# Optimization experiments

Measured on AMD Instinct MI355X. Metric: run time of the kernel, lower is better.

The kernel has to match this reference:

```python
import jax, jax.numpy as jnp
import numpy as np

C = 2000        # num_classes
D_FEAT = 2048   # memory feature dim (hardcoded in module)
N_V = 20000     # rgb samples
N_I = 20000     # ir samples
T = 1.0
PRED_W, FEAT_W, CONF_W = 0.45, 0.4, 0.15
OT_REG, OT_ITERS = 0.07, 30
HIGH_TH, MID_TH, TOPK = 0.55, 0.25, 3


def setup_inputs() -> dict:
    key = jax.random.key(0)
    k = jax.random.split(key, 6)
    return {
        "vis_logits": jax.random.normal(k[0], (N_V, C), jnp.float32),
        "ir_logits": jax.random.normal(k[1], (N_I, C), jnp.float32),
        "vis_memory": jax.random.normal(k[2], (C, D_FEAT), jnp.float32),
        "ir_memory": jax.random.normal(k[3], (C, D_FEAT), jnp.float32),
        "rgb_ids": jax.random.randint(k[4], (N_V,), 0, C),
        "ir_ids": jax.random.randint(k[5], (N_I,), 0, C),
    }


def _class_stats(scores, labels):
    # per-class mean of softmax scores + entropy (matches _build_class_stats)
    proto_sum = jax.ops.segment_sum(scores, labels, num_segments=C)      # [C, C]
    counts = jax.ops.segment_sum(jnp.ones((scores.shape[0],), scores.dtype), labels, num_segments=C)
    proto = proto_sum / jnp.clip(counts, 1.0)[:, None]
    p = jnp.clip(proto, 1e-12)
    entropy = -(p * jnp.log(p)).sum(axis=1)
    return proto, counts, entropy, counts > 0


def _sinkhorn(cost, a, b, mask_f):
    kernel = jnp.exp(-cost / max(OT_REG, 1e-4)) * mask_f
    eps = 1e-8
    def body(_, uv):
        u, v = uv
        kv = kernel @ v + eps
        u = jnp.where(a > 0, a / kv, 0.0)
        ktu = kernel.T @ u + eps
        v = jnp.where(b > 0, b / ktu, 0.0)
        return (u, v)
    u, v = jax.lax.fori_loop(0, OT_ITERS, body, (jnp.ones_like(a), jnp.ones_like(b)))
    return u[:, None] * kernel * v[None, :] * mask_f


def _topk_mask(m):
    k = min(TOPK, m.shape[1])
    vals, idx = jax.lax.top_k(m, k)
    rows = jnp.arange(m.shape[0])[:, None]
    return jnp.zeros_like(m).at[rows, idx].set(vals)


def reference(vis_logits, ir_logits, vis_memory, ir_memory, rgb_ids, ir_ids):
    # save() in 'scores' mode: temperature softmax
    vis_scores = jax.nn.softmax(T * vis_logits, axis=1)
    ir_scores = jax.nn.softmax(T * ir_logits, axis=1)

    vis_proto, vis_count, vis_ent, vis_active = _class_stats(vis_scores, rgb_ids)
    ir_proto, ir_count, ir_ent, ir_active = _class_stats(ir_scores, ir_ids)

    vmem = vis_memory / jnp.clip(jnp.linalg.norm(vis_memory, axis=1, keepdims=True), 1e-12)
    imem = ir_memory / jnp.clip(jnp.linalg.norm(ir_memory, axis=1, keepdims=True), 1e-12)
    feat_score = jnp.clip((vmem @ imem.T + 1.0) * 0.5, 0.0, 1.0)          # [C, C]
    pred_score = 0.5 * (vis_proto + ir_proto.T)
    conf_score = jnp.clip(
        1.0 - (vis_ent[:, None] + ir_ent[None, :]) / (2.0 * np.log(C + 1e-12)), 0.0, 1.0)

    active = vis_active[:, None] & ir_active[None, :]
    cost = PRED_W * (1.0 - pred_score) + FEAT_W * (1.0 - feat_score) + CONF_W * (1.0 - conf_score)
    masked_max = jnp.max(jnp.where(active, cost, -jnp.inf))
    high = jnp.where(active.any(), masked_max + 1.0, 1.0)
    cost = jnp.where(active, cost, high)

    a = vis_count / jnp.clip(vis_count.sum(), 1.0)
    b = ir_count / jnp.clip(ir_count.sum(), 1.0)
    transport = _sinkhorn(cost, a, b, active.astype(cost.dtype))

    row_t = transport / jnp.clip(transport.sum(axis=1, keepdims=True), 1e-12)
    col_t = transport.T / jnp.clip(transport.T.sum(axis=1, keepdims=True), 1e-12)
    row_conf = row_t.max(axis=1); row_assign = row_t.argmax(axis=1)
    col_conf = col_t.max(axis=1); col_assign = col_t.argmax(axis=1)

    ids = jnp.arange(C)
    mutual_rows = col_assign[row_assign] == ids
    mutual_cols = row_assign[col_assign] == ids
    common_row = vis_active & (row_conf >= HIGH_TH) & mutual_rows
    common_col = ir_active & (col_conf >= HIGH_TH) & mutual_cols
    spec_row = vis_active & (row_conf >= HIGH_TH) & ~common_row
    rem_row = vis_active & (row_conf >= MID_TH) & (row_conf < HIGH_TH)
    rem_col = ir_active & (col_conf >= MID_TH) & (col_conf < HIGH_TH)

    common_rm = jnp.where(common_row[:, None],
                          jax.nn.one_hot(row_assign, C, dtype=row_t.dtype) * row_conf[:, None],
                          0.0)
    specific_rm = row_t * spec_row[:, None].astype(row_t.dtype)
    remain_rm = _topk_mask(row_t * rem_row[:, None].astype(row_t.dtype))
    remain_col_rm = _topk_mask(col_t * rem_col[:, None].astype(col_t.dtype))

    return jnp.stack([row_t, col_t, common_rm, specific_rm, remain_rm, remain_col_rm])
```

## Files before the change

### kernel.cpp

```cpp
#include <hip/hip_runtime.h>

#define CN 2000
#define DF 2048
#define NS 20000
#define NBLK 250
#define NGRP 25
#define GRPSZ 10

typedef __attribute__((ext_vector_type(4))) float          f32x4;
typedef __attribute__((ext_vector_type(4))) int            i32x4;
typedef __attribute__((ext_vector_type(4))) unsigned short u16x4;

__device__ __forceinline__ float wredSum(float v){
#pragma unroll
  for (int o = 32; o >= 1; o >>= 1) v += __shfl_xor(v, o, 64);
  return v;
}
__device__ __forceinline__ float wredMax(float v){
#pragma unroll
  for (int o = 32; o >= 1; o >>= 1) v = fmaxf(v, __shfl_xor(v, o, 64));
  return v;
}
__device__ __forceinline__ unsigned short bfbits(float x){
  union { float f; unsigned u; } c; c.f = x;
  return (unsigned short)((c.u + 0x7fffu + ((c.u >> 16) & 1u)) >> 16);
}
__device__ __forceinline__ void gload16(const void* g, void* lds){
  __builtin_amdgcn_global_load_lds((const __attribute__((address_space(1))) unsigned int*)g,
      (__attribute__((address_space(3))) unsigned int*)lds, 16, 0, 0);
}

__device__ __forceinline__ void gbar(int* bar, int target){
  asm volatile("s_waitcnt vmcnt(0)" ::: "memory");
  __syncthreads();
  if (threadIdx.x == 0){
    int g = blockIdx.x / GRPSZ;
    int prev = __hip_atomic_fetch_add(&bar[64 + g * 32], 1,
                  __ATOMIC_RELAXED, __HIP_MEMORY_SCOPE_AGENT);
    if (prev == target * GRPSZ - 1){
      int rp = __hip_atomic_fetch_add(&bar[0], 1,
                  __ATOMIC_RELAXED, __HIP_MEMORY_SCOPE_AGENT);
      if (rp == target * NGRP - 1){
        __hip_atomic_store(&bar[32], target, __ATOMIC_RELAXED, __HIP_MEMORY_SCOPE_AGENT);
      }
    }
    while (__hip_atomic_load(&bar[32], __ATOMIC_RELAXED, __HIP_MEMORY_SCOPE_AGENT) < target){
      __builtin_amdgcn_s_sleep(2);
    }
  }
  __syncthreads();
}

__global__ void k_zero(int* p, int n, int* bar){
  int i = blockIdx.x * 256 + threadIdx.x;
  if (i < n) p[i] = 0;
  if (i < 1024) bar[i] = 0;
}

__global__ void k_hist(const int* __restrict__ rgb, const int* __restrict__ iri,
                       int* cv, int* ci){
  int i = blockIdx.x * 256 + threadIdx.x;
  if (i < NS) atomicAdd(&cv[rgb[i]], 1);
  else if (i < 2 * NS) atomicAdd(&ci[iri[i - NS]], 1);
}

__global__ __launch_bounds__(1024) void k_scan(const int* __restrict__ cv, const int* __restrict__ ci,
                                               int* ov, int* oi){
  __shared__ int s[2048];
  int t = threadIdx.x;
  for (int pass = 0; pass < 2; ++pass){
    const int* c = pass ? ci : cv;
    int* o = pass ? oi : ov;
    s[t] = (t < CN) ? c[t] : 0;
    s[t + 1024] = (t + 1024 < CN) ? c[t + 1024] : 0;
    __syncthreads();
    for (int off = 1; off < 2048; off <<= 1){
      int a = (t >= off) ? s[t - off] : 0;
      int b = (t + 1024 >= off) ? s[t + 1024 - off] : 0;
      __syncthreads();
      s[t] += a; s[t + 1024] += b;
      __syncthreads();
    }
    if (t < CN) o[t] = s[t] - c[t];
    if (t + 1024 < CN) o[t + 1024] = s[t + 1024] - c[t + 1024];
    __syncthreads();
  }
}

__global__ void k_scatter(const int* __restrict__ rgb, const int* __restrict__ iri,
                          const int* __restrict__ ov, const int* __restrict__ oi,
                          int* curv, int* curi, int* ordv, int* ordi){
  int i = blockIdx.x * 256 + threadIdx.x;
  if (i < NS){
    int l = rgb[i];
    int p = atomicAdd(&curv[l], 1);
    ordv[ov[l] + p] = i;
  } else if (i < 2 * NS){
    int k = i - NS;
    int l = iri[k];
    int p = atomicAdd(&curi[l], 1);
    ordi[oi[l] + p] = k;
  }
}

__global__ __launch_bounds__(256) void k_class(const float* __restrict__ visl, const float* __restrict__ irl,
    const int* __restrict__ cv, const int* __restrict__ ci,
    const int* __restrict__ ov, const int* __restrict__ oi,
    const int* __restrict__ ordv, const int* __restrict__ ordi,
    float* __restrict__ pv, float* __restrict__ pi_,
    float* __restrict__ ev, float* __restrict__ ei){
  __shared__ __attribute__((aligned(16))) float acc4[4][2048];
  __shared__ int mem[128];
  __shared__ float red[4];
  int t = threadIdx.x, w = t >> 6, l = t & 63;
  bool ir = (blockIdx.x >= CN);
  int c = ir ? blockIdx.x - CN : blockIdx.x;
  const float* logits = ir ? irl : visl;
  int n = (ir ? ci : cv)[c];
  int base = (ir ? oi : ov)[c];
  const int* ord = ir ? ordi : ordv;
  float* proto = ir ? pi_ : pv;
  float* ent = ir ? ei : ev;
  bool useL = (n <= 128);
  for (int m = t; m < n && m < 128; m += 256) mem[m] = ord[base + m];
  for (int j = t; j < 2048; j += 256){
    acc4[0][j] = 0.f; acc4[1][j] = 0.f; acc4[2][j] = 0.f; acc4[3][j] = 0.f;
  }
  __syncthreads();
  if (t == 0 && useL){
    for (int a = 1; a < n; ++a){
      int key = mem[a]; int b = a - 1;
      while (b >= 0 && mem[b] > key){ mem[b + 1] = mem[b]; --b; }
      mem[b + 1] = key;
    }
  }
  __syncthreads();
  for (int m = w; m < n; m += 4){
    int sidx = useL ? mem[m] : ord[base + m];
    const f32x4* row = (const f32x4*)(logits + (size_t)sidx * CN);
    f32x4 x[8]; float mx = -3.0e38f;
#pragma unroll
    for (int k = 0; k < 8; ++k){
      int idx = l + k * 64;
      f32x4 vv = {-3.0e38f, -3.0e38f, -3.0e38f, -3.0e38f};
      if (idx < 500) vv = row[idx];
      x[k] = vv;
      mx = fmaxf(mx, fmaxf(fmaxf(vv[0], vv[1]), fmaxf(vv[2], vv[3])));
    }
    mx = wredMax(mx);
    float sm = 0.f;
#pragma unroll
    for (int k = 0; k < 8; ++k){
      int idx = l + k * 64;
      if (idx < 500){
        f32x4 e;
        e[0] = expf(x[k][0] - mx); e[1] = expf(x[k][1] - mx);
        e[2] = expf(x[k][2] - mx); e[3] = expf(x[k][3] - mx);
        x[k] = e;
        sm += e[0] + e[1] + e[2] + e[3];
      }
    }
    sm = wredSum(sm);
    float inv = 1.f / sm;
#pragma unroll
    for (int k = 0; k < 8; ++k){
      int idx = l + k * 64;
      if (idx < 500){
        f32x4* a = (f32x4*)&acc4[w][idx * 4];
        f32x4 cur = *a;
        cur[0] += x[k][0] * inv; cur[1] += x[k][1] * inv;
        cur[2] += x[k][2] * inv; cur[3] += x[k][3] * inv;
        *a = cur;
      }
    }
  }
  __syncthreads();
  float invc = 1.f / fmaxf((float)n, 1.f);
  float el = 0.f;
  for (int j = t; j < CN; j += 256){
    float p = (acc4[0][j] + acc4[1][j] + acc4[2][j] + acc4[3][j]) * invc;
    proto[(size_t)c * CN + j] = p;
    p = fmaxf(p, 1e-12f);
    el -= p * logf(p);
  }
  el = wredSum(el);
  if (l == 0) red[w] = el;
  __syncthreads();
  if (t == 0) ent[c] = red[0] + red[1] + red[2] + red[3];
}

__global__ __launch_bounds__(256) void k_conv(const float* __restrict__ vm, const float* __restrict__ im,
    unsigned short* __restrict__ vmb, unsigned short* __restrict__ imb,
    float* __restrict__ rv, float* __restrict__ ri){
  int g = blockIdx.x * 256 + threadIdx.x;
  int wid = g >> 6, l = g & 63;
  if (wid >= 2 * CN) return;
  const float* src = (wid < CN) ? vm : im;
  unsigned short* dst = (wid < CN) ? vmb : imb;
  int r = (wid < CN) ? wid : wid - CN;
  const f32x4* row = (const f32x4*)(src + (size_t)r * DF);
  float s = 0.f;
#pragma unroll
  for (int k = 0; k < 8; ++k){
    int idx = l + k * 64;
    f32x4 vv = row[idx];
    s += vv[0]*vv[0] + vv[1]*vv[1] + vv[2]*vv[2] + vv[3]*vv[3];
    u16x4 o;
    o[0] = bfbits(vv[0]); o[1] = bfbits(vv[1]); o[2] = bfbits(vv[2]); o[3] = bfbits(vv[3]);
    *(u16x4*)(dst + (size_t)r * DF + idx * 4) = o;
  }
  s = wredSum(s);
  if (l == 0) ((wid < CN) ? rv : ri)[r] = 1.f / fmaxf(sqrtf(s), 1e-12f);
}

__global__ __launch_bounds__(256) void k_prep(const float* __restrict__ pv, const float* __restrict__ pi_,
    const float* __restrict__ ev, const float* __restrict__ ei,
    const int* __restrict__ cv, const int* __restrict__ ci, float* __restrict__ E){
  __shared__ float s[64][65];
  int t = threadIdx.x;
  int i0 = blockIdx.y * 64, j0 = blockIdx.x * 64;
#pragma unroll
  for (int rr = 0; rr < 4; ++rr){
    int jl = (t >> 4) + rr * 16;
    int ch = t & 15;
    int gj = j0 + jl;
    int gib = i0 + ch * 4;
    f32x4 vv = {0.f, 0.f, 0.f, 0.f};
    if (gj < CN){
      if (gib + 3 < CN) vv = *(const f32x4*)(pi_ + (size_t)gj * CN + gib);
      else {
        for (int q = 0; q < 4; ++q) if (gib + q < CN) vv[q] = pi_[(size_t)gj * CN + gib + q];
      }
    }
    s[ch*4+0][jl] = vv[0]; s[ch*4+1][jl] = vv[1]; s[ch*4+2][jl] = vv[2]; s[ch*4+3][jl] = vv[3];
  }
  __syncthreads();
#pragma unroll
  for (int rr = 0; rr < 4; ++rr){
    int il = (t >> 4) + rr * 16;
    int ch = t & 15;
    int gi = i0 + il;
    int gjb = j0 + ch * 4;
    if (gi >= CN) continue;
    f32x4 pvv = {0.f, 0.f, 0.f, 0.f};
    bool full = (gjb + 3 < CN);
    if (full) pvv = *(const f32x4*)(pv + (size_t)gi * CN + gjb);
    else { for (int q = 0; q < 4; ++q) if (gjb + q < CN) pvv[q] = pv[(size_t)gi * CN + gjb + q]; }
    float evi = ev[gi];
    bool avi = cv[gi] > 0;
    f32x4 o;
#pragma unroll
    for (int q = 0; q < 4; ++q){
      int gj = gjb + q;
      if (gj >= CN){ o[q] = 0.f; continue; }
      float pred = 0.5f * (pvv[q] + s[il][ch*4+q]);
      float conf = fminf(fmaxf(1.f - (evi + ei[gj]) / 15.201804919084164f, 0.f), 1.f);
      float base = 0.45f * (1.f - pred) + 0.15f * (1.f - conf);
      bool act = avi && (ci[gj] > 0);
      o[q] = act ? expf(-base / 0.07f) : 0.f;
    }
    if (full) *(f32x4*)(E + (size_t)gi * CN + gjb) = o;
    else { for (int q = 0; q < 4; ++q) if (gjb + q < CN) E[(size_t)gi * CN + gjb + q] = o[q]; }
  }
}

__global__ __launch_bounds__(256) void k_gemm2(const unsigned short* __restrict__ Ag,
    const unsigned short* __restrict__ Bg, const float* __restrict__ rv,
    const float* __restrict__ ri, const float* __restrict__ E, float* __restrict__ Km){
  __shared__ __attribute__((aligned(16))) unsigned short As[128 * 64];
  __shared__ __attribute__((aligned(16))) unsigned short Bs[128 * 64];
  int t = threadIdx.x, w = t >> 6, l = t & 63;
  int i0 = blockIdx.y * 128, j0 = blockIdx.x * 128;
  int wm = w >> 1, wn = w & 1;
  int srow8 = l >> 3, sch = l & 7;
  int lr = l & 15, hk = l >> 4;
  f32x4 z = {0.f, 0.f, 0.f, 0.f};
  f32x4 acc[4][4];
#pragma unroll
  for (int a = 0; a < 4; ++a)
#pragma unroll
    for (int b = 0; b < 4; ++b) acc[a][b] = z;

  for (int kt = 0; kt < DF / 64; ++kt){
    int k0 = kt * 64;
#pragma unroll
    for (int c2 = 0; c2 < 4; ++c2){
      int rbase = c2 * 32 + w * 8;
      int row = rbase + srow8;
      int lch = sch ^ (srow8 & 7);
      int gi = i0 + row; if (gi > CN - 1) gi = CN - 1;
      int gj = j0 + row; if (gj > CN - 1) gj = CN - 1;
      gload16(Ag + (size_t)gi * DF + k0 + lch * 8, &As[rbase * 64]);
      gload16(Bg + (size_t)gj * DF + k0 + lch * 8, &Bs[rbase * 64]);
    }
    __syncthreads();
#pragma unroll
    for (int s2 = 0; s2 < 2; ++s2){
      i32x4 af[4], bf[4];
#pragma unroll
      for (int f2 = 0; f2 < 4; ++f2){
        int ar = wm * 64 + f2 * 16 + lr;
        int ac = (s2 * 4 + hk) ^ (ar & 7);
        af[f2] = *(const i32x4*)&As[ar * 64 + ac * 8];
        int br = wn * 64 + f2 * 16 + lr;
        int bc = (s2 * 4 + hk) ^ (br & 7);
        bf[f2] = *(const i32x4*)&Bs[br * 64 + bc * 8];
      }
#pragma unroll
      for (int a = 0; a < 4; ++a)
#pragma unroll
        for (int b = 0; b < 4; ++b)
          asm volatile("v_mfma_f32_16x16x32_bf16 %0, %1, %2, %0"
                       : "+v"(acc[a][b]) : "v"(af[a]), "v"(bf[b]));
    }
    __syncthreads();
  }
#pragma unroll
  for (int a = 0; a < 4; ++a){
    int ib = i0 + wm * 64 + a * 16 + hk * 4;
#pragma unroll
    for (int b = 0; b < 4; ++b){
      int j = j0 + wn * 64 + b * 16 + lr;
      if (j < CN){
        float rij = ri[j];
#pragma unroll
        for (int q = 0; q < 4; ++q){
          int i = ib + q;
          if (i < CN){
            float dot = acc[a][b][q] * rv[i] * rij;
            float feat = fminf(fmaxf((dot + 1.f) * 0.5f, 0.f), 1.f);
            float kv = E[(size_t)i * CN + j] * expf(-0.4f * (1.f - feat) / 0.07f);
            Km[(size_t)i * CN + j] = kv;
          }
        }
      }
    }
  }
}

__global__ __launch_bounds__(256) void k_tr(const float* __restrict__ Km, float* __restrict__ KT){
  __shared__ float s[64][65];
  int t = threadIdx.x;
  int i0 = blockIdx.y * 64, j0 = blockIdx.x * 64;
#pragma unroll
  for (int rr = 0; rr < 4; ++rr){
    int il = (t >> 4) + rr * 16;
    int ch = t & 15;
    int gi = i0 + il, gjb = j0 + ch * 4;
    f32x4 vv = {0.f, 0.f, 0.f, 0.f};
    if (gi < CN){
      if (gjb + 3 < CN) vv = *(const f32x4*)(Km + (size_t)gi * CN + gjb);
      else { for (int q = 0; q < 4; ++q) if (gjb + q < CN) vv[q] = Km[(size_t)gi * CN + gjb + q]; }
    }
    s[ch*4+0][il] = vv[0]; s[ch*4+1][il] = vv[1]; s[ch*4+2][il] = vv[2]; s[ch*4+3][il] = vv[3];
  }
  __syncthreads();
#pragma unroll
  for (int rr = 0; rr < 4; ++rr){
    int jl = (t >> 4) + rr * 16;
    int ch = t & 15;
    int gj = j0 + jl, gib = i0 + ch * 4;
    if (gj >= CN) continue;
    f32x4 o;
    o[0] = s[jl][ch*4+0]; o[1] = s[jl][ch*4+1]; o[2] = s[jl][ch*4+2]; o[3] = s[jl][ch*4+3];
    if (gib + 3 < CN) *(f32x4*)(KT + (size_t)gj * CN + gib) = o;
    else { for (int q = 0; q < 4; ++q) if (gib + q < CN) KT[(size_t)gj * CN + gib + q] = o[q]; }
  }
}

__global__ __launch_bounds__(256, 1) void k_sink(
    const float* __restrict__ Km, const float* __restrict__ KTm,
    const int* __restrict__ cv, const int* __restrict__ ci,
    float* __restrict__ u_g, float* __restrict__ v_g,
    float* __restrict__ o0, float* __restrict__ o1,
    float* __restrict__ rconf, float* __restrict__ cconf,
    int* __restrict__ rass, int* __restrict__ cass,
    int* bar){
  __shared__ __attribute__((aligned(16))) float u_lds[2000];
  __shared__ __attribute__((aligned(16))) float v_lds[2000];
  int b = blockIdx.x, t = threadIdx.x, w = t >> 6, l = t & 63;
  int r0 = b * 8 + w * 2, r1 = r0 + 1;
  f32x4 z4 = {0.f, 0.f, 0.f, 0.f};
  f32x4 kA0[8], kA1[8], kT0[8], kT1[8];
  {
    const f32x4* g0 = (const f32x4*)(Km + (size_t)r0 * CN);
    const f32x4* g1 = (const f32x4*)(Km + (size_t)r1 * CN);
    const f32x4* h0 = (const f32x4*)(KTm + (size_t)r0 * CN);
    const f32x4* h1 = (const f32x4*)(KTm + (size_t)r1 * CN);
#pragma unroll
    for (int k = 0; k < 8; ++k){
      int idx = l + k * 64;
      bool ok = idx < 500;
      kA0[k] = ok ? g0[idx] : z4;
      kA1[k] = ok ? g1[idx] : z4;
      kT0[k] = ok ? h0[idx] : z4;
      kT1[k] = ok ? h1[idx] : z4;
    }
  }
  float a0 = (float)cv[r0] / 20000.0f, a1 = (float)cv[r1] / 20000.0f;
  float b0 = (float)ci[r0] / 20000.0f, b1 = (float)ci[r1] / 20000.0f;

  {
    float s0 = 0.f, s1 = 0.f;
#pragma unroll
    for (int k = 0; k < 8; ++k){
      s0 += kA0[k][0] + kA0[k][1] + kA0[k][2] + kA0[k][3];
      s1 += kA1[k][0] + kA1[k][1] + kA1[k][2] + kA1[k][3];
    }
    s0 = wredSum(s0); s1 = wredSum(s1);
    if (l == 0){
      __hip_atomic_store(&u_g[r0], (a0 > 0.f) ? a0 / (s0 + 1e-8f) : 0.f,
                         __ATOMIC_RELAXED, __HIP_MEMORY_SCOPE_AGENT);
      __hip_atomic_store(&u_g[r1], (a1 > 0.f) ? a1 / (s1 + 1e-8f) : 0.f,
                         __ATOMIC_RELAXED, __HIP_MEMORY_SCOPE_AGENT);
    }
  }
  int tgt = 1;
  gbar(bar, tgt); ++tgt;
  {
    float tmp[8];
#pragma unroll
    for (int k = 0; k < 8; ++k){
      int idx = t + k * 256;
      tmp[k] = (idx < CN) ? __hip_atomic_load(&u_g[idx], __ATOMIC_RELAXED, __HIP_MEMORY_SCOPE_AGENT) : 0.f;
    }
#pragma unroll
    for (int k = 0; k < 8; ++k){ int idx = t + k * 256; if (idx < CN) u_lds[idx] = tmp[k]; }
  }
  __syncthreads();
  const f32x4* ul4 = (const f32x4*)u_lds;
  const f32x4* vl4 = (const f32x4*)v_lds;

  for (int it = 0; it < 30; ++it){
    {
      float s0 = 0.f, s1 = 0.f;
#pragma unroll
      for (int k = 0; k < 8; ++k){
        int idx = l + k * 64;
        if (idx < 500){
          f32x4 x = ul4[idx];
          s0 += kT0[k][0]*x[0] + kT0[k][1]*x[1] + kT0[k][2]*x[2] + kT0[k][3]*x[3];
          s1 += kT1[k][0]*x[0] + kT1[k][1]*x[1] + kT1[k][2]*x[2] + kT1[k][3]*x[3];
        }
      }
      s0 = wredSum(s0); s1 = wredSum(s1);
      if (l == 0){
        __hip_atomic_store(&v_g[r0], (b0 > 0.f) ? b0 / (s0 + 1e-8f) : 0.f,
                           __ATOMIC_RELAXED, __HIP_MEMORY_SCOPE_AGENT);
        __hip_atomic_store(&v_g[r1], (b1 > 0.f) ? b1 / (s1 + 1e-8f) : 0.f,
                           __ATOMIC_RELAXED, __HIP_MEMORY_SCOPE_AGENT);
      }
    }
    gbar(bar, tgt); ++tgt;
    {
      float tmp[8];
#pragma unroll
      for (int k = 0; k < 8; ++k){
        int idx = t + k * 256;
        tmp[k] = (idx < CN) ? __hip_atomic_load(&v_g[idx], __ATOMIC_RELAXED, __HIP_MEMORY_SCOPE_AGENT) : 0.f;
      }
#pragma unroll
      for (int k = 0; k < 8; ++k){ int idx = t + k * 256; if (idx < CN) v_lds[idx] = tmp[k]; }
    }
    __syncthreads();
    if (it < 29){
      {
        float s0 = 0.f, s1 = 0.f;
#pragma unroll
        for (int k = 0; k < 8; ++k){
          int idx = l + k * 64;
          if (idx < 500){
            f32x4 x = vl4[idx];
            s0 += kA0[k][0]*x[0] + kA0[k][1]*x[1] + kA0[k][2]*x[2] + kA0[k][3]*x[3];
            s1 += kA1[k][0]*x[0] + kA1[k][1]*x[1] + kA1[k][2]*x[2] + kA1[k][3]*x[3];
          }
        }
        s0 = wredSum(s0); s1 = wredSum(s1);
        if (l == 0){
          __hip_atomic_store(&u_g[r0], (a0 > 0.f) ? a0 / (s0 + 1e-8f) : 0.f,
                             __ATOMIC_RELAXED, __HIP_MEMORY_SCOPE_AGENT);
          __hip_atomic_store(&u_g[r1], (a1 > 0.f) ? a1 / (s1 + 1e-8f) : 0.f,
                             __ATOMIC_RELAXED, __HIP_MEMORY_SCOPE_AGENT);
        }
      }
      gbar(bar, tgt); ++tgt;
      {
        float tmp[8];
#pragma unroll
        for (int k = 0; k < 8; ++k){
          int idx = t + k * 256;
          tmp[k] = (idx < CN) ? __hip_atomic_load(&u_g[idx], __ATOMIC_RELAXED, __HIP_MEMORY_SCOPE_AGENT) : 0.f;
        }
#pragma unroll
        for (int k = 0; k < 8; ++k){ int idx = t + k * 256; if (idx < CN) u_lds[idx] = tmp[k]; }
      }
      __syncthreads();
    }
  }
  {
    float s0 = 0.f, s1 = 0.f;
#pragma unroll
    for (int k = 0; k < 8; ++k){
      int idx = l + k * 64;
      if (idx < 500){
        f32x4 x = vl4[idx];
        s0 += kA0[k][0]*x[0] + kA0[k][1]*x[1] + kA0[k][2]*x[2] + kA0[k][3]*x[3];
        s1 += kA1[k][0]*x[0] + kA1[k][1]*x[1] + kA1[k][2]*x[2] + kA1[k][3]*x[3];
      }
    }
    s0 = wredSum(s0); s1 = wredSum(s1);
    float uu0 = u_lds[r0], uu1 = u_lds[r1];
    float f0 = uu0 * (1.f / fmaxf(uu0 * s0, 1e-12f));
    float f1 = uu1 * (1.f / fmaxf(uu1 * s1, 1e-12f));
    float bm0 = -1e30f, bm1 = -1e30f; int bi0 = 1 << 30, bi1 = 1 << 30;
    f32x4* d0 = (f32x4*)(o0 + (size_t)r0 * CN);
    f32x4* d1 = (f32x4*)(o0 + (size_t)r1 * CN);
#pragma unroll
    for (int k = 0; k < 8; ++k){
      int idx = l + k * 64;
      if (idx < 500){
        f32x4 x = vl4[idx];
        f32x4 w0, w1;
#pragma unroll
        for (int q = 0; q < 4; ++q){
          w0[q] = f0 * kA0[k][q] * x[q];
          w1[q] = f1 * kA1[k][q] * x[q];
        }
        d0[idx] = w0; d1[idx] = w1;
#pragma unroll
        for (int q = 0; q < 4; ++q){
          int j = idx * 4 + q;
          if (w0[q] > bm0){ bm0 = w0[q]; bi0 = j; }
          if (w1[q] > bm1){ bm1 = w1[q]; bi1 = j; }
        }
      }
    }
#pragma unroll
    for (int o = 32; o >= 1; o >>= 1){
      float om = __shfl_xor(bm0, o, 64); int oi2 = __shfl_xor(bi0, o, 64);
      if (om > bm0 || (om == bm0 && oi2 < bi0)){ bm0 = om; bi0 = oi2; }
      float om1 = __shfl_xor(bm1, o, 64); int oi3 = __shfl_xor(bi1, o, 64);
      if (om1 > bm1 || (om1 == bm1 && oi3 < bi1)){ bm1 = om1; bi1 = oi3; }
    }
    if (l == 0){ rconf[r0] = bm0; rass[r0] = bi0; rconf[r1] = bm1; rass[r1] = bi1; }
  }
  {
    float s0 = 0.f, s1 = 0.f;
#pragma unroll
    for (int k = 0; k < 8; ++k){
      int idx = l + k * 64;
      if (idx < 500){
        f32x4 x = ul4[idx];
        s0 += kT0[k][0]*x[0] + kT0[k][1]*x[1] + kT0[k][2]*x[2] + kT0[k][3]*x[3];
        s1 += kT1[k][0]*x[0] + kT1[k][1]*x[1] + kT1[k][2]*x[2] + kT1[k][3]*x[3];
      }
    }
    s0 = wredSum(s0); s1 = wredSum(s1);
    float vv0 = v_lds[r0], vv1 = v_lds[r1];
    float f0 = vv0 * (1.f / fmaxf(vv0 * s0, 1e-12f));
    float f1 = vv1 * (1.f / fmaxf(vv1 * s1, 1e-12f));
    float bm0 = -1e30f, bm1 = -1e30f; int bi0 = 1 << 30, bi1 = 1 << 30;
    f32x4* d0 = (f32x4*)(o1 + (size_t)r0 * CN);
    f32x4* d1 = (f32x4*)(o1 + (size_t)r1 * CN);
#pragma unroll
    for (int k = 0; k < 8; ++k){
      int idx = l + k * 64;
      if (idx < 500){
        f32x4 x = ul4[idx];
        f32x4 w0, w1;
#pragma unroll
        for (int q = 0; q < 4; ++q){
          w0[q] = f0 * kT0[k][q] * x[q];
          w1[q] = f1 * kT1[k][q] * x[q];
        }
        d0[idx] = w0; d1[idx] = w1;
#pragma unroll
        for (int q = 0; q < 4; ++q){
          int j = idx * 4 + q;
          if (w0[q] > bm0){ bm0 = w0[q]; bi0 = j; }
          if (w1[q] > bm1){ bm1 = w1[q]; bi1 = j; }
        }
      }
    }
#pragma unroll
    for (int o = 32; o >= 1; o >>= 1){
      float om = __shfl_xor(bm0, o, 64); int oi2 = __shfl_xor(bi0, o, 64);
      if (om > bm0 || (om == bm0 && oi2 < bi0)){ bm0 = om; bi0 = oi2; }
      float om1 = __shfl_xor(bm1, o, 64); int oi3 = __shfl_xor(bi1, o, 64);
      if (om1 > bm1 || (om1 == bm1 && oi3 < bi1)){ bm1 = om1; bi1 = oi3; }
    }
    if (l == 0){ cconf[r0] = bm0; cass[r0] = bi0; cconf[r1] = bm1; cass[r1] = bi1; }
  }
}

__global__ __launch_bounds__(256) void k_fill(const float* __restrict__ rt,
    const int* __restrict__ cv, const float* __restrict__ rc,
    const int* __restrict__ ra, const int* __restrict__ ca,
    float* o2, float* o3, float* o4, float* o5){
  int i = blockIdx.x, t = threadIdx.x;
  bool av = cv[i] > 0;
  float cval = rc[i]; int aidx = ra[i];
  bool high = av && (cval >= 0.55f);
  bool cm = high && (ca[aidx] == i);
  bool sp = high && !cm;
  f32x4 z = {0.f, 0.f, 0.f, 0.f};
  f32x4* p2 = (f32x4*)(o2 + (size_t)i * CN);
  f32x4* p3 = (f32x4*)(o3 + (size_t)i * CN);
  f32x4* p4 = (f32x4*)(o4 + (size_t)i * CN);
  f32x4* p5 = (f32x4*)(o5 + (size_t)i * CN);
  const f32x4* rp = (const f32x4*)(rt + (size_t)i * CN);
  for (int c = t; c < 500; c += 256){
    p2[c] = z;
    p3[c] = sp ? rp[c] : z;
    p4[c] = z;
    p5[c] = z;
  }
  __syncthreads();
  if (t == 0 && cm) o2[(size_t)i * CN + aidx] = cval;
}

__global__ __launch_bounds__(256) void k_topk(const float* __restrict__ rt, const float* __restrict__ ct,
    const int* __restrict__ cv, const int* __restrict__ ci,
    const float* __restrict__ rc, const float* __restrict__ cc,
    float* o4, float* o5){
  __shared__ float sv[256 * 3];
  __shared__ int si[256 * 3];
  int b = blockIdx.x;
  bool colp = (b >= CN);
  int r = colp ? b - CN : b;
  bool act = colp ? (ci[r] > 0) : (cv[r] > 0);
  float cf = colp ? cc[r] : rc[r];
  if (!(act && cf >= 0.25f && cf < 0.55f)) return;
  const float* M = colp ? ct : rt;
  float* o = colp ? o5 : o4;
  int t = threadIdx.x;
  float v0 = -1.f, v1 = -1.f, v2 = -1.f;
  int i0 = 1 << 30, i1 = 1 << 30, i2 = 1 << 30;
  for (int k = 0; k < 8; ++k){
    int j = t + k * 256;
    if (j >= CN) break;
    float val = M[(size_t)r * CN + j];
    if (val > v0 || (val == v0 && j < i0)){ v2=v1; i2=i1; v1=v0; i1=i0; v0=val; i0=j; }
    else if (val > v1 || (val == v1 && j < i1)){ v2=v1; i2=i1; v1=val; i1=j; }
    else if (val > v2 || (val == v2 && j < i2)){ v2=val; i2=j; }
  }
  sv[t*3+0]=v0; sv[t*3+1]=v1; sv[t*3+2]=v2;
  si[t*3+0]=i0; si[t*3+1]=i1; si[t*3+2]=i2;
  __syncthreads();
  if (t == 0){
    float w0=-1.f, w1=-1.f, w2=-1.f; int j0=1<<30, j1=1<<30, j2=1<<30;
    for (int q = 0; q < 256 * 3; ++q){
      float val = sv[q]; int j = si[q];
      if (j >= CN) continue;
      if (val > w0 || (val == w0 && j < j0)){ w2=w1; j2=j1; w1=w0; j1=j0; w0=val; j0=j; }
      else if (val > w1 || (val == w1 && j < j1)){ w2=w1; j2=j1; w1=val; j1=j; }
      else if (val > w2 || (val == w2 && j < j2)){ w2=val; j2=j; }
    }
    o[(size_t)r * CN + j0] = w0;
    o[(size_t)r * CN + j1] = w1;
    o[(size_t)r * CN + j2] = w2;
  }
}

extern "C" void kernel_launch(void* const* d_in, const int* in_sizes, int n_in,
                              void* d_out, int out_size, void* d_ws, size_t ws_size,
                              hipStream_t stream){
  (void)in_sizes; (void)n_in; (void)out_size; (void)ws_size;
  const float* visl = (const float*)d_in[0];
  const float* irl  = (const float*)d_in[1];
  const float* vm   = (const float*)d_in[2];
  const float* im   = (const float*)d_in[3];
  const int* rgb    = (const int*)d_in[4];
  const int* iri    = (const int*)d_in[5];
  float* out = (float*)d_out;
  float* o0 = out;
  float* o1 = out + 4000000;
  float* o2 = out + 8000000;
  float* o3 = out + 12000000;
  float* o4 = out + 16000000;
  float* o5 = out + 20000000;
  char* sm = (char*)d_ws;
  float* ev   = (float*)(sm + 0);
  float* ei   = (float*)(sm + 8000);
  float* rv   = (float*)(sm + 16000);
  float* ri   = (float*)(sm + 24000);
  float* uvec = (float*)(sm + 32000);
  float* vvec = (float*)(sm + 40000);
  int* bar    = (int*)(sm + 48000);
  float* rconf= (float*)(sm + 64000);
  float* cconf= (float*)(sm + 72000);
  int* rass = (int*)(sm + 80000);
  int* cass = (int*)(sm + 88000);
  int* cv   = (int*)(sm + 96000);
  int* ci   = (int*)(sm + 104000);
  int* ov   = (int*)(sm + 112000);
  int* oi   = (int*)(sm + 120000);
  int* curv = (int*)(sm + 128000);
  int* curi = (int*)(sm + 136000);
  int* ordv = (int*)(sm + 176000);
  int* ordi = (int*)(sm + 256000);
  unsigned short* vmb = (unsigned short*)o2;
  unsigned short* imb = (unsigned short*)o3;

  k_zero<<<47, 256, 0, stream>>>(cv, 12000, bar);
  k_hist<<<157, 256, 0, stream>>>(rgb, iri, cv, ci);
  k_scan<<<1, 1024, 0, stream>>>(cv, ci, ov, oi);
  k_scatter<<<157, 256, 0, stream>>>(rgb, iri, ov, oi, curv, curi, ordv, ordi);
  k_class<<<2 * CN, 256, 0, stream>>>(visl, irl, cv, ci, ov, oi, ordv, ordi, o2, o3, ev, ei);
  k_prep<<<dim3(32, 32), 256, 0, stream>>>(o2, o3, ev, ei, cv, ci, o4);
  k_conv<<<1000, 256, 0, stream>>>(vm, im, vmb, imb, rv, ri);
  k_gemm2<<<dim3(16, 16), 256, 0, stream>>>(vmb, imb, rv, ri, o4, o0);
  k_tr<<<dim3(32, 32), 256, 0, stream>>>(o0, o1);
  k_sink<<<NBLK, 256, 0, stream>>>(o0, o1, cv, ci, uvec, vvec, o0, o1,
                                   rconf, cconf, rass, cass, bar);
  k_fill<<<CN, 256, 0, stream>>>(o0, cv, rconf, rass, cass, o2, o3, o4, o5);
  k_topk<<<2 * CN, 256, 0, stream>>>(o0, o1, cv, ci, rconf, cconf, o4, o5);
}
```

Baseline: 429.7 us.

## Fuse memory conversion into class kernel, merge fill/topk, halve sinkhorn block count

The bf16 conversion of the memory banks now runs as extra blocks of the class-statistics kernel, and the fill and top-k kernels are merged into one post-processing kernel. This removes two launches and lets the conversion overlap with the class reduction. The persistent Sinkhorn kernel now uses 125 blocks of 512 threads instead of 250 of 256, which halves the number of participants in each grid barrier, and the barrier spin sleep is shortened. The bf16 scratch buffers move to the o5/o1 output slices so they do not collide with o2/o3, which are still written by the class kernel running alongside.

```diff
diff --git a/kernel.cpp b/kernel.cpp
--- a/kernel.cpp
+++ b/kernel.cpp
@@ -3,9 +3,9 @@
 #define CN 2000
 #define DF 2048
 #define NS 20000
-#define NBLK 250
+#define NBLK 125
 #define NGRP 25
-#define GRPSZ 10
+#define GRPSZ 5
 
 typedef __attribute__((ext_vector_type(4))) float          f32x4;
 typedef __attribute__((ext_vector_type(4))) int            i32x4;
@@ -45,7 +45,7 @@
       }
     }
     while (__hip_atomic_load(&bar[32], __ATOMIC_RELAXED, __HIP_MEMORY_SCOPE_AGENT) < target){
-      __builtin_amdgcn_s_sleep(2);
+      __builtin_amdgcn_s_sleep(1);
     }
   }
   __syncthreads();
@@ -108,7 +108,32 @@
     const int* __restrict__ ov, const int* __restrict__ oi,
     const int* __restrict__ ordv, const int* __restrict__ ordi,
     float* __restrict__ pv, float* __restrict__ pi_,
-    float* __restrict__ ev, float* __restrict__ ei){
+    float* __restrict__ ev, float* __restrict__ ei,
+    const float* __restrict__ vm, const float* __restrict__ im,
+    unsigned short* __restrict__ vmb, unsigned short* __restrict__ imb,
+    float* __restrict__ rv, float* __restrict__ ri){
+  if (blockIdx.x >= 2 * CN){
+    int g = (blockIdx.x - 2 * CN) * 256 + threadIdx.x;
+    int wid = g >> 6, l = g & 63;
+    if (wid >= 2 * CN) return;
+    const float* src = (wid < CN) ? vm : im;
+    unsigned short* dst = (wid < CN) ? vmb : imb;
+    int r = (wid < CN) ? wid : wid - CN;
+    const f32x4* row = (const f32x4*)(src + (size_t)r * DF);
+    float s = 0.f;
+#pragma unroll
+    for (int k = 0; k < 8; ++k){
+      int idx = l + k * 64;
+      f32x4 vv = row[idx];
+      s += vv[0]*vv[0] + vv[1]*vv[1] + vv[2]*vv[2] + vv[3]*vv[3];
+      u16x4 o;
+      o[0] = bfbits(vv[0]); o[1] = bfbits(vv[1]); o[2] = bfbits(vv[2]); o[3] = bfbits(vv[3]);
+      *(u16x4*)(dst + (size_t)r * DF + idx * 4) = o;
+    }
+    s = wredSum(s);
+    if (l == 0) ((wid < CN) ? rv : ri)[r] = 1.f / fmaxf(sqrtf(s), 1e-12f);
+    return;
+  }
   __shared__ __attribute__((aligned(16))) float acc4[4][2048];
   __shared__ int mem[128];
   __shared__ float red[4];
@@ -189,30 +214,6 @@
   if (t == 0) ent[c] = red[0] + red[1] + red[2] + red[3];
 }
 
-__global__ __launch_bounds__(256) void k_conv(const float* __restrict__ vm, const float* __restrict__ im,
-    unsigned short* __restrict__ vmb, unsigned short* __restrict__ imb,
-    float* __restrict__ rv, float* __restrict__ ri){
-  int g = blockIdx.x * 256 + threadIdx.x;
-  int wid = g >> 6, l = g & 63;
-  if (wid >= 2 * CN) return;
-  const float* src = (wid < CN) ? vm : im;
-  unsigned short* dst = (wid < CN) ? vmb : imb;
-  int r = (wid < CN) ? wid : wid - CN;
-  const f32x4* row = (const f32x4*)(src + (size_t)r * DF);
-  float s = 0.f;
-#pragma unroll
-  for (int k = 0; k < 8; ++k){
-    int idx = l + k * 64;
-    f32x4 vv = row[idx];
-    s += vv[0]*vv[0] + vv[1]*vv[1] + vv[2]*vv[2] + vv[3]*vv[3];
-    u16x4 o;
-    o[0] = bfbits(vv[0]); o[1] = bfbits(vv[1]); o[2] = bfbits(vv[2]); o[3] = bfbits(vv[3]);
-    *(u16x4*)(dst + (size_t)r * DF + idx * 4) = o;
-  }
-  s = wredSum(s);
-  if (l == 0) ((wid < CN) ? rv : ri)[r] = 1.f / fmaxf(sqrtf(s), 1e-12f);
-}
-
 __global__ __launch_bounds__(256) void k_prep(const float* __restrict__ pv, const float* __restrict__ pi_,
     const float* __restrict__ ev, const float* __restrict__ ei,
     const int* __restrict__ cv, const int* __restrict__ ci, float* __restrict__ E){
@@ -368,7 +369,18 @@
   }
 }
 
-__global__ __launch_bounds__(256, 1) void k_sink(
+#define STAGE(G, L) do { \
+  float tmp_[4]; \
+  _Pragma("unroll") \
+  for (int k_ = 0; k_ < 4; ++k_){ \
+    int idx_ = t + k_ * 512; \
+    tmp_[k_] = (idx_ < CN) ? __hip_atomic_load(&(G)[idx_], __ATOMIC_RELAXED, __HIP_MEMORY_SCOPE_AGENT) : 0.f; \
+  } \
+  _Pragma("unroll") \
+  for (int k_ = 0; k_ < 4; ++k_){ int idx_ = t + k_ * 512; if (idx_ < CN) (L)[idx_] = tmp_[k_]; } \
+} while(0)
+
+__global__ __launch_bounds__(512, 1) void k_sink(
     const float* __restrict__ Km, const float* __restrict__ KTm,
     const int* __restrict__ cv, const int* __restrict__ ci,
     float* __restrict__ u_g, float* __restrict__ v_g,
@@ -376,10 +388,10 @@
     float* __restrict__ rconf, float* __restrict__ cconf,
     int* __restrict__ rass, int* __restrict__ cass,
     int* bar){
-  __shared__ __attribute__((aligned(16))) float u_lds[2000];
-  __shared__ __attribute__((aligned(16))) float v_lds[2000];
+  __shared__ __attribute__((aligned(16))) float u_lds[2048];
+  __shared__ __attribute__((aligned(16))) float v_lds[2048];
   int b = blockIdx.x, t = threadIdx.x, w = t >> 6, l = t & 63;
-  int r0 = b * 8 + w * 2, r1 = r0 + 1;
+  int r0 = b * 16 + w * 2, r1 = r0 + 1;
   f32x4 z4 = {0.f, 0.f, 0.f, 0.f};
   f32x4 kA0[8], kA1[8], kT0[8], kT1[8];
   {
@@ -417,16 +429,7 @@
   }
   int tgt = 1;
   gbar(bar, tgt); ++tgt;
-  {
-    float tmp[8];
-#pragma unroll
-    for (int k = 0; k < 8; ++k){
-      int idx = t + k * 256;
-      tmp[k] = (idx < CN) ? __hip_atomic_load(&u_g[idx], __ATOMIC_RELAXED, __HIP_MEMORY_SCOPE_AGENT) : 0.f;
-    }
-#pragma unroll
-    for (int k = 0; k < 8; ++k){ int idx = t + k * 256; if (idx < CN) u_lds[idx] = tmp[k]; }
-  }
+  STAGE(u_g, u_lds);
   __syncthreads();
   const f32x4* ul4 = (const f32x4*)u_lds;
   const f32x4* vl4 = (const f32x4*)v_lds;
@@ -452,16 +455,7 @@
       }
     }
     gbar(bar, tgt); ++tgt;
-    {
-      float tmp[8];
-#pragma unroll
-      for (int k = 0; k < 8; ++k){
-        int idx = t + k * 256;
-        tmp[k] = (idx < CN) ? __hip_atomic_load(&v_g[idx], __ATOMIC_RELAXED, __HIP_MEMORY_SCOPE_AGENT) : 0.f;
-      }
-#pragma unroll
-      for (int k = 0; k < 8; ++k){ int idx = t + k * 256; if (idx < CN) v_lds[idx] = tmp[k]; }
-    }
+    STAGE(v_g, v_lds);
     __syncthreads();
     if (it < 29){
       {
@@ -484,16 +478,7 @@
         }
       }
       gbar(bar, tgt); ++tgt;
-      {
-        float tmp[8];
-#pragma unroll
-        for (int k = 0; k < 8; ++k){
-          int idx = t + k * 256;
-          tmp[k] = (idx < CN) ? __hip_atomic_load(&u_g[idx], __ATOMIC_RELAXED, __HIP_MEMORY_SCOPE_AGENT) : 0.f;
-        }
-#pragma unroll
-        for (int k = 0; k < 8; ++k){ int idx = t + k * 256; if (idx < CN) u_lds[idx] = tmp[k]; }
-      }
+      STAGE(u_g, u_lds);
       __syncthreads();
     }
   }
@@ -593,16 +578,22 @@
   }
 }
 
-__global__ __launch_bounds__(256) void k_fill(const float* __restrict__ rt,
-    const int* __restrict__ cv, const float* __restrict__ rc,
+__global__ __launch_bounds__(256) void k_post(const float* __restrict__ rt, const float* __restrict__ ct,
+    const int* __restrict__ cv, const int* __restrict__ ci,
+    const float* __restrict__ rc, const float* __restrict__ cc,
     const int* __restrict__ ra, const int* __restrict__ ca,
     float* o2, float* o3, float* o4, float* o5){
+  __shared__ float sv[256 * 3];
+  __shared__ int si[256 * 3];
   int i = blockIdx.x, t = threadIdx.x;
-  bool av = cv[i] > 0;
-  float cval = rc[i]; int aidx = ra[i];
-  bool high = av && (cval >= 0.55f);
+  bool av = cv[i] > 0, ai = ci[i] > 0;
+  float rcv = rc[i], ccv = cc[i];
+  int aidx = ra[i];
+  bool high = av && (rcv >= 0.55f);
   bool cm = high && (ca[aidx] == i);
   bool sp = high && !cm;
+  bool remr = av && (rcv >= 0.25f) && (rcv < 0.55f);
+  bool remc = ai && (ccv >= 0.25f) && (ccv < 0.55f);
   f32x4 z = {0.f, 0.f, 0.f, 0.f};
   f32x4* p2 = (f32x4*)(o2 + (size_t)i * CN);
   f32x4* p3 = (f32x4*)(o3 + (size_t)i * CN);
@@ -616,49 +607,39 @@
     p5[c] = z;
   }
   __syncthreads();
-  if (t == 0 && cm) o2[(size_t)i * CN + aidx] = cval;
-}
-
-__global__ __launch_bounds__(256) void k_topk(const float* __restrict__ rt, const float* __restrict__ ct,
-    const int* __restrict__ cv, const int* __restrict__ ci,
-    const float* __restrict__ rc, const float* __restrict__ cc,
-    float* o4, float* o5){
-  __shared__ float sv[256 * 3];
-  __shared__ int si[256 * 3];
-  int b = blockIdx.x;
-  bool colp = (b >= CN);
-  int r = colp ? b - CN : b;
-  bool act = colp ? (ci[r] > 0) : (cv[r] > 0);
-  float cf = colp ? cc[r] : rc[r];
-  if (!(act && cf >= 0.25f && cf < 0.55f)) return;
-  const float* M = colp ? ct : rt;
-  float* o = colp ? o5 : o4;
-  int t = threadIdx.x;
-  float v0 = -1.f, v1 = -1.f, v2 = -1.f;
-  int i0 = 1 << 30, i1 = 1 << 30, i2 = 1 << 30;
-  for (int k = 0; k < 8; ++k){
-    int j = t + k * 256;
-    if (j >= CN) break;
-    float val = M[(size_t)r * CN + j];
-    if (val > v0 || (val == v0 && j < i0)){ v2=v1; i2=i1; v1=v0; i1=i0; v0=val; i0=j; }
-    else if (val > v1 || (val == v1 && j < i1)){ v2=v1; i2=i1; v1=val; i1=j; }
-    else if (val > v2 || (val == v2 && j < i2)){ v2=val; i2=j; }
-  }
-  sv[t*3+0]=v0; sv[t*3+1]=v1; sv[t*3+2]=v2;
-  si[t*3+0]=i0; si[t*3+1]=i1; si[t*3+2]=i2;
-  __syncthreads();
-  if (t == 0){
-    float w0=-1.f, w1=-1.f, w2=-1.f; int j0=1<<30, j1=1<<30, j2=1<<30;
-    for (int q = 0; q < 256 * 3; ++q){
-      float val = sv[q]; int j = si[q];
-      if (j >= CN) continue;
-      if (val > w0 || (val == w0 && j < j0)){ w2=w1; j2=j1; w1=w0; j1=j0; w0=val; j0=j; }
-      else if (val > w1 || (val == w1 && j < j1)){ w2=w1; j2=j1; w1=val; j1=j; }
-      else if (val > w2 || (val == w2 && j < j2)){ w2=val; j2=j; }
-    }
-    o[(size_t)r * CN + j0] = w0;
-    o[(size_t)r * CN + j1] = w1;
-    o[(size_t)r * CN + j2] = w2;
+  if (t == 0 && cm) o2[(size_t)i * CN + aidx] = rcv;
+  for (int pass = 0; pass < 2; ++pass){
+    bool run = pass ? remc : remr;
+    if (!run) continue;
+    const float* M = pass ? ct : rt;
+    float* o = pass ? o5 : o4;
+    float v0 = -1.f, v1 = -1.f, v2 = -1.f;
+    int i0 = 1 << 30, i1 = 1 << 30, i2 = 1 << 30;
+    for (int k = 0; k < 8; ++k){
+      int j = t + k * 256;
+      if (j >= CN) break;
+      float val = M[(size_t)i * CN + j];
+      if (val > v0 || (val == v0 && j < i0)){ v2=v1; i2=i1; v1=v0; i1=i0; v0=val; i0=j; }
+      else if (val > v1 || (val == v1 && j < i1)){ v2=v1; i2=i1; v1=val; i1=j; }
+      else if (val > v2 || (val == v2 && j < i2)){ v2=val; i2=j; }
+    }
+    sv[t*3+0]=v0; sv[t*3+1]=v1; sv[t*3+2]=v2;
+    si[t*3+0]=i0; si[t*3+1]=i1; si[t*3+2]=i2;
+    __syncthreads();
+    if (t == 0){
+      float w0=-1.f, w1=-1.f, w2=-1.f; int j0=1<<30, j1=1<<30, j2=1<<30;
+      for (int q = 0; q < 256 * 3; ++q){
+        float val = sv[q]; int j = si[q];
+        if (j >= CN) continue;
+        if (val > w0 || (val == w0 && j < j0)){ w2=w1; j2=j1; w1=w0; j1=j0; w0=val; j0=j; }
+        else if (val > w1 || (val == w1 && j < j1)){ w2=w1; j2=j1; w1=val; j1=j; }
+        else if (val > w2 || (val == w2 && j < j2)){ w2=val; j2=j; }
+      }
+      o[(size_t)i * CN + j0] = w0;
+      o[(size_t)i * CN + j1] = w1;
+      o[(size_t)i * CN + j2] = w2;
+    }
+    __syncthreads();
   }
 }
 
@@ -699,20 +680,19 @@
   int* curi = (int*)(sm + 136000);
   int* ordv = (int*)(sm + 176000);
   int* ordi = (int*)(sm + 256000);
-  unsigned short* vmb = (unsigned short*)o2;
-  unsigned short* imb = (unsigned short*)o3;
+  unsigned short* vmb = (unsigned short*)o5;
+  unsigned short* imb = (unsigned short*)o1;
 
   k_zero<<<47, 256, 0, stream>>>(cv, 12000, bar);
   k_hist<<<157, 256, 0, stream>>>(rgb, iri, cv, ci);
   k_scan<<<1, 1024, 0, stream>>>(cv, ci, ov, oi);
   k_scatter<<<157, 256, 0, stream>>>(rgb, iri, ov, oi, curv, curi, ordv, ordi);
-  k_class<<<2 * CN, 256, 0, stream>>>(visl, irl, cv, ci, ov, oi, ordv, ordi, o2, o3, ev, ei);
+  k_class<<<2 * CN + 1000, 256, 0, stream>>>(visl, irl, cv, ci, ov, oi, ordv, ordi,
+                                             o2, o3, ev, ei, vm, im, vmb, imb, rv, ri);
   k_prep<<<dim3(32, 32), 256, 0, stream>>>(o2, o3, ev, ei, cv, ci, o4);
-  k_conv<<<1000, 256, 0, stream>>>(vm, im, vmb, imb, rv, ri);
   k_gemm2<<<dim3(16, 16), 256, 0, stream>>>(vmb, imb, rv, ri, o4, o0);
   k_tr<<<dim3(32, 32), 256, 0, stream>>>(o0, o1);
-  k_sink<<<NBLK, 256, 0, stream>>>(o0, o1, cv, ci, uvec, vvec, o0, o1,
+  k_sink<<<NBLK, 512, 0, stream>>>(o0, o1, cv, ci, uvec, vvec, o0, o1,
                                    rconf, cconf, rass, cass, bar);
-  k_fill<<<CN, 256, 0, stream>>>(o0, cv, rconf, rass, cass, o2, o3, o4, o5);
-  k_topk<<<2 * CN, 256, 0, stream>>>(o0, o1, cv, ci, rconf, cconf, o4, o5);
-}
+  k_post<<<CN, 256, 0, stream>>>(o0, o1, cv, ci, rconf, cconf, rass, cass, o2, o3, o4, o5);
+}
```

After: 423.2 us. About the same (-1.5%).
